# Kernel tuning notes

Measured on AMD Instinct MI355X. Metric: run time of the kernel, lower is better.

## Reference

```python
import jax, jax.numpy as jnp
import numpy as np

B, S, D = 4, 2048, 768   # batch, seq_len, dim_inp
H, E = 12, 64            # num_heads, dim_out (per-head)
LN_EPS = 1e-5


def setup_inputs() -> dict:
    key = jax.random.key(0)
    ks = jax.random.split(key, 12)
    sd = 1.0 / np.sqrt(D)
    x = jax.random.normal(ks[0], (B, S, D), dtype=jnp.float32)
    Wq = jax.random.normal(ks[1], (H, D, E), dtype=jnp.float32) * sd
    bq = jax.random.normal(ks[2], (H, E), dtype=jnp.float32) * 0.02
    Wk = jax.random.normal(ks[3], (H, D, E), dtype=jnp.float32) * sd
    bk = jax.random.normal(ks[4], (H, E), dtype=jnp.float32) * 0.02
    Wv = jax.random.normal(ks[5], (H, D, E), dtype=jnp.float32) * sd
    bv = jax.random.normal(ks[6], (H, E), dtype=jnp.float32) * 0.02
    Wo = jax.random.normal(ks[7], (H * E, D), dtype=jnp.float32) * (1.0 / np.sqrt(H * E))
    bo = jax.random.normal(ks[8], (D,), dtype=jnp.float32) * 0.02
    gamma = jnp.ones((D,), dtype=jnp.float32)
    beta = jnp.zeros((D,), dtype=jnp.float32)
    return {"input_tensor": x, "Wq": Wq, "bq": bq, "Wk": Wk, "bk": bk,
            "Wv": Wv, "bv": bv, "Wo": Wo, "bo": bo, "gamma": gamma, "beta": beta}


def reference(input_tensor, Wq, bq, Wk, bk, Wv, bv, Wo, bo, gamma, beta):
    x = input_tensor  # [B,S,D]
    # all heads at once: [B,H,S,E]
    q = jnp.einsum('bsd,hde->bhse', x, Wq) + bq[None, :, None, :]
    k = jnp.einsum('bsd,hde->bhse', x, Wk) + bk[None, :, None, :]
    v = jnp.einsum('bsd,hde->bhse', x, Wv) + bv[None, :, None, :]
    # NOTE: original divides by sqrt(seq_len) (query.size(1)), not sqrt(head_dim)
    scale = jnp.sqrt(jnp.float32(q.shape[2]))
    scores = jnp.einsum('bhse,bhte->bhst', q, k) / scale  # [B,H,S,S]
    attn = jax.nn.softmax(scores, axis=-1)
    ctx = jnp.einsum('bhst,bhte->bhse', attn, v)          # [B,H,S,E]
    # concat heads along last dim: [B,S,H*E]
    ctx = ctx.transpose(0, 2, 1, 3).reshape(x.shape[0], x.shape[1], -1)
    proj = ctx @ Wo + bo                                   # [B,S,D]
    h = x + proj
    mu = jnp.mean(h, axis=-1, keepdims=True)
    var = jnp.mean(jnp.square(h - mu), axis=-1, keepdims=True)
    y = (h - mu) * jax.lax.rsqrt(var + LN_EPS) * gamma + beta
    return y
```

## Files before the change

### kernel.cpp

```cpp
#include <hip/hip_runtime.h>


typedef __bf16 bf16x8 __attribute__((ext_vector_type(8)));
typedef __bf16 bf16x4 __attribute__((ext_vector_type(4)));
typedef float  f32x4  __attribute__((ext_vector_type(4)));
typedef float  f32x16 __attribute__((ext_vector_type(16)));
typedef unsigned u32x4 __attribute__((ext_vector_type(4)));

#define MFMA16(a,b,c) __builtin_amdgcn_mfma_f32_16x16x32_bf16((a),(b),(c),0,0,0)
#define MFMA32(a,b,c) __builtin_amdgcn_mfma_f32_32x32x16_bf16((a),(b),(c),0,0,0)
#define QSCALE2 (0.022097086912079612f * 1.4426950408889634f)

__device__ __forceinline__ void gload16(const void* g, void* l) {
  __builtin_amdgcn_global_load_lds((const __attribute__((address_space(1))) void*)g,
                                   (__attribute__((address_space(3))) void*)l, 16, 0, 0);
}

__global__ __launch_bounds__(256) void pack_kernel(
    const float* __restrict__ x, const float* __restrict__ Wq,
    const float* __restrict__ Wk, const float* __restrict__ Wv,
    const float* __restrict__ Wo,
    __bf16* __restrict__ xb, __bf16* __restrict__ wqkv, __bf16* __restrict__ wot) {
  int tid = blockIdx.x * 256 + threadIdx.x;
  int nth = gridDim.x * 256;
  for (int i = tid; i < 8192 * 768 / 4; i += nth) {
    float4 v = ((const float4*)x)[i];
    bf16x4 o; o[0] = (__bf16)v.x; o[1] = (__bf16)v.y; o[2] = (__bf16)v.z; o[3] = (__bf16)v.w;
    ((bf16x4*)xb)[i] = o;
  }
  for (int i = tid; i < 3 * 768 * 768; i += nth) {
    int n = i / 768, d = i - n * 768;
    int p = n / 768;
    int wn = n - p * 768;
    int h = wn >> 6, e = wn & 63;
    const float* W = (p == 0) ? Wq : (p == 1) ? Wk : Wv;
    wqkv[i] = (__bf16)W[(h * 768 + d) * 64 + e];
  }
  for (int i = tid; i < 768 * 768; i += nth) {
    int n = i / 768, k = i - n * 768;
    wot[i] = (__bf16)Wo[k * 768 + n];
  }
}

#define GEMM_CORE(A_, Bt_, m0_, n0_)                                              \
  __shared__ __bf16 As[128 * 32];                                                 \
  __shared__ __bf16 Bs[128 * 32];                                                 \
  const int tid = threadIdx.x;                                                    \
  const int w = tid >> 6, lane = tid & 63, ln = lane & 15, hi = lane >> 4;        \
  const int wr = w >> 1, wc = w & 1;                                              \
  f32x4 acc[4][4];                                                                \
  {                                                                               \
    f32x4 z = {0.f, 0.f, 0.f, 0.f};                                               \
    _Pragma("unroll") for (int i = 0; i < 4; ++i)                                 \
      _Pragma("unroll") for (int j = 0; j < 4; ++j) acc[i][j] = z;                \
  }                                                                               \
  {                                                                               \
    const int r0 = tid >> 2, cc = (tid & 3) * 8;                                  \
    const __bf16* ga0 = A_ + (size_t)(m0_ + r0) * 768 + cc;                       \
    const __bf16* ga1 = A_ + (size_t)(m0_ + 64 + r0) * 768 + cc;                  \
    const __bf16* gb0 = Bt_ + (size_t)(n0_ + r0) * 768 + cc;                      \
    const __bf16* gb1 = Bt_ + (size_t)(n0_ + 64 + r0) * 768 + cc;                 \
    __bf16* la0 = &As[w * 512];                                                   \
    __bf16* la1 = &As[2048 + w * 512];                                            \
    __bf16* lb0 = &Bs[w * 512];                                                   \
    __bf16* lb1 = &Bs[2048 + w * 512];                                            \
    for (int kt = 0; kt < 24; ++kt) {                                             \
      const int kk = kt * 32;                                                     \
      gload16(ga0 + kk, la0);                                                     \
      gload16(ga1 + kk, la1);                                                     \
      gload16(gb0 + kk, lb0);                                                     \
      gload16(gb1 + kk, lb1);                                                     \
      __syncthreads();                                                            \
      bf16x8 af[4], bfv[4];                                                       \
      _Pragma("unroll") for (int mt = 0; mt < 4; ++mt)                            \
        af[mt] = *(const bf16x8*)&As[(wr * 64 + mt * 16 + ln) * 32 + hi * 8];     \
      _Pragma("unroll") for (int nt = 0; nt < 4; ++nt)                            \
        bfv[nt] = *(const bf16x8*)&Bs[(wc * 64 + nt * 16 + ln) * 32 + hi * 8];    \
      _Pragma("unroll") for (int mt = 0; mt < 4; ++mt)                            \
        _Pragma("unroll") for (int nt = 0; nt < 4; ++nt)                          \
          acc[mt][nt] = MFMA16(af[mt], bfv[nt], acc[mt][nt]);                     \
      __syncthreads();                                                            \
    }                                                                             \
  }

__global__ __launch_bounds__(256) void gemm_qkv(
    const __bf16* __restrict__ A, const __bf16* __restrict__ Bt,
    const float* __restrict__ bq, const float* __restrict__ bk,
    const float* __restrict__ bv,
    __bf16* __restrict__ qb, __bf16* __restrict__ kb, __bf16* __restrict__ vt) {
  const int lin = blockIdx.y * 18 + blockIdx.x;
  const int swzb = (lin & 7) * 144 + (lin >> 3);
  const int m0 = (swzb / 18) * 128, n0 = (swzb % 18) * 128;
  GEMM_CORE(A, Bt, m0, n0)
  const int p = n0 / 768;
  const float* bias = (p == 0) ? bq : (p == 1) ? bk : bv;
  const float sc = (p == 0) ? QSCALE2 : 1.0f;
#pragma unroll
  for (int nt = 0; nt < 4; ++nt) {
    int n = n0 + wc * 64 + nt * 16 + ln;
    int wn = n - p * 768;
    int h = wn >> 6, e = wn & 63;
    float bb = bias[wn];
#pragma unroll
    for (int mt = 0; mt < 4; ++mt) {
      int mrow = m0 + wr * 64 + mt * 16 + hi * 4;
      int b = mrow >> 11, s0 = mrow & 2047;
      if (p == 2) {
        bf16x4 pk;
#pragma unroll
        for (int r = 0; r < 4; ++r) pk[r] = (__bf16)(acc[mt][nt][r] + bb);
        *(bf16x4*)&vt[(((size_t)b * 12 + h) * 64 + e) * 2048 + s0] = pk;
      } else {
        __bf16* dst = (p == 0) ? qb : kb;
#pragma unroll
        for (int r = 0; r < 4; ++r)
          dst[(((size_t)b * 12 + h) * 2048 + s0 + r) * 64 + e] =
              (__bf16)((acc[mt][nt][r] + bb) * sc);
      }
    }
  }
}

__global__ __launch_bounds__(256) void gemm_proj(
    const __bf16* __restrict__ A, const __bf16* __restrict__ Bt,
    const float* __restrict__ bo, const float* __restrict__ xres,
    float* __restrict__ hout) {
  const int lin = blockIdx.y * 6 + blockIdx.x;
  const int swzb = (lin & 7) * 48 + (lin >> 3);
  const int m0 = (swzb / 6) * 128, n0 = (swzb % 6) * 128;
  GEMM_CORE(A, Bt, m0, n0)
#pragma unroll
  for (int nt = 0; nt < 4; ++nt) {
    int n = n0 + wc * 64 + nt * 16 + ln;
    float bb = bo[n];
#pragma unroll
    for (int mt = 0; mt < 4; ++mt) {
      int mrow = m0 + wr * 64 + mt * 16 + hi * 4;
#pragma unroll
      for (int r = 0; r < 4; ++r) {
        size_t idx = (size_t)(mrow + r) * 768 + n;
        hout[idx] = acc[mt][nt][r] + bb + xres[idx];
      }
    }
  }
}

__global__ __launch_bounds__(256, 3) void attn_kernel(
    const __bf16* __restrict__ qb, const __bf16* __restrict__ kb,
    const __bf16* __restrict__ vt, __bf16* __restrict__ ctx) {
  __shared__ __align__(16) char lds[32768];
  const int tid = threadIdx.x;
  const int w = tid >> 6, lane = tid & 63;
  const int l31 = lane & 31, h = lane >> 5;
  const int lin = blockIdx.x * 16 + blockIdx.y;
  const int swzb = (lin & 7) * 96 + (lin >> 3);
  const int bh = swzb >> 4;
  const int q0 = (swzb & 15) * 128 + w * 32;

  const int o0 = tid * 16, o1 = o0 + 4096;
  const int r0s = o0 >> 7, cb0 = o0 & 127;
  const int r1s = o1 >> 7, cb1 = o1 & 127;
  const char* kgb = (const char*)(kb + (size_t)bh * 2048 * 64);
  const char* vgb = (const char*)(vt + (size_t)bh * 64 * 2048);
  const char* ksrc0 = kgb + r0s * 128 + (cb0 ^ ((r0s & 7) << 4));
  const char* ksrc1 = kgb + r1s * 128 + (cb1 ^ ((r1s & 7) << 4));
  const char* vsrc0 = vgb + r0s * 4096 + (cb0 ^ ((r0s & 7) << 4));
  const char* vsrc1 = vgb + r1s * 4096 + (cb1 ^ ((r1s & 7) << 4));
  char* kl0 = lds + w * 1024;
  char* vl0 = lds + 16384 + w * 1024;

#define STAGE(t_, b_) do {                                   \
    gload16(ksrc0 + (size_t)(t_) * 8192, kl0 + (b_) * 8192); \
    gload16(ksrc1 + (size_t)(t_) * 8192, kl0 + (b_) * 8192 + 4096); \
    gload16(vsrc0 + (size_t)(t_) * 128,  vl0 + (b_) * 8192); \
    gload16(vsrc1 + (size_t)(t_) * 128,  vl0 + (b_) * 8192 + 4096); \
  } while (0)

  const __bf16* qp = qb + ((size_t)bh * 2048 + q0 + l31) * 64 + h * 8;
  bf16x8 qf[4];
#pragma unroll
  for (int s = 0; s < 4; ++s) qf[s] = *(const bf16x8*)(qp + 16 * s);

  const int swz = (l31 & 7) << 4;
  const int krd = l31 * 128 + ((h * 16) ^ swz);
  const int vrd = 16384 + l31 * 128 + ((h * 16) ^ swz);

  float ls0 = 0.f, ls1 = 0.f, ls2 = 0.f, ls3 = 0.f;
  f32x16 cacc[2];
#pragma unroll
  for (int et = 0; et < 2; ++et)
#pragma unroll
    for (int r = 0; r < 16; ++r) cacc[et][r] = 0.f;

  STAGE(0, 0);
  __syncthreads();
  int buf = 0;

  for (int t = 0; t < 32; ++t) {
    if (t < 31) STAGE(t + 1, buf ^ 1);
    const char* kb_l = lds + buf * 8192;
    bf16x8 kf[2][4], vf[4][2];
#pragma unroll
    for (int kvt = 0; kvt < 2; ++kvt)
#pragma unroll
      for (int s = 0; s < 4; ++s)
        kf[kvt][s] = *(const bf16x8*)(kb_l + ((krd + kvt * 4096) ^ (s * 32)));
#pragma unroll
    for (int ks = 0; ks < 4; ++ks) {
      vf[ks][0] = *(const bf16x8*)(kb_l + ((vrd + 0 * 4096) ^ (ks * 32)));
      vf[ks][1] = *(const bf16x8*)(kb_l + ((vrd + 1 * 4096) ^ (ks * 32)));
    }
    u32x4 pau[4];
#pragma unroll
    for (int kvt = 0; kvt < 2; ++kvt) {
      f32x16 sa;
#pragma unroll
      for (int r = 0; r < 16; ++r) sa[r] = 0.f;
      __builtin_amdgcn_s_setprio(1);
#pragma unroll
      for (int s = 0; s < 4; ++s) sa = MFMA32(kf[kvt][s], qf[s], sa);
      __builtin_amdgcn_s_setprio(0);
      unsigned c0, c1, c2, c3, c4, c5, c6, c7;
#define PKPAIR(dst_, i_, ls_)                                                \
      {                                                                      \
        float pa_ = __builtin_amdgcn_exp2f(sa[2 * (i_)]);                    \
        float pb_ = __builtin_amdgcn_exp2f(sa[2 * (i_) + 1]);                \
        ls_ += pa_ + pb_;                                                    \
        asm("v_cvt_pk_bf16_f32 %0, %1, %2" : "=v"(dst_) : "v"(pa_), "v"(pb_)); \
      }
      PKPAIR(c0, 0, ls0) PKPAIR(c1, 1, ls1) PKPAIR(c2, 2, ls2) PKPAIR(c3, 3, ls3)
      PKPAIR(c4, 4, ls0) PKPAIR(c5, 5, ls1) PKPAIR(c6, 6, ls2) PKPAIR(c7, 7, ls3)
#undef PKPAIR
      asm("v_permlane32_swap_b32 %0, %1" : "+v"(c0), "+v"(c2));
      asm("v_permlane32_swap_b32 %0, %1" : "+v"(c1), "+v"(c3));
      asm("v_permlane32_swap_b32 %0, %1" : "+v"(c4), "+v"(c6));
      asm("v_permlane32_swap_b32 %0, %1" : "+v"(c5), "+v"(c7));
      pau[2 * kvt][0] = c0; pau[2 * kvt][1] = c1;
      pau[2 * kvt][2] = c2; pau[2 * kvt][3] = c3;
      pau[2 * kvt + 1][0] = c4; pau[2 * kvt + 1][1] = c5;
      pau[2 * kvt + 1][2] = c6; pau[2 * kvt + 1][3] = c7;
    }
    __builtin_amdgcn_s_setprio(1);
#pragma unroll
    for (int ks = 0; ks < 4; ++ks) {
      bf16x8 paf = __builtin_bit_cast(bf16x8, pau[ks]);
      cacc[0] = MFMA32(paf, vf[ks][0], cacc[0]);
      cacc[1] = MFMA32(paf, vf[ks][1], cacc[1]);
    }
    __builtin_amdgcn_s_setprio(0);
    __syncthreads();
    buf ^= 1;
  }
#undef STAGE

  float lsum = (ls0 + ls1) + (ls2 + ls3);
  lsum += __shfl_xor(lsum, 32, 64);
  float inv = 1.0f / lsum;
  const int b = bh / 12, hh = bh - b * 12;
#pragma unroll
  for (int r = 0; r < 16; ++r) {
    const int ql = (r & 3) + 8 * (r >> 2) + 4 * h;
    float rl = __shfl(inv, ql, 64);
    size_t base = ((size_t)b * 2048 + q0 + ql) * 768 + hh * 64 + l31;
    ctx[base]      = (__bf16)(cacc[0][r] * rl);
    ctx[base + 32] = (__bf16)(cacc[1][r] * rl);
  }
}

__global__ __launch_bounds__(256) void ln_kernel(
    const float* __restrict__ hb, const float* __restrict__ gamma,
    const float* __restrict__ beta, float* __restrict__ out) {
  __shared__ float ssum[4], ssq[4];
  const int row = blockIdx.x, t = threadIdx.x;
  const float* hr = hb + (size_t)row * 768;
  float v0 = hr[t], v1 = hr[t + 256], v2 = hr[t + 512];
  float sum = v0 + v1 + v2;
  float sq = v0 * v0 + v1 * v1 + v2 * v2;
#pragma unroll
  for (int mask = 1; mask < 64; mask <<= 1) {
    sum += __shfl_xor(sum, mask, 64);
    sq += __shfl_xor(sq, mask, 64);
  }
  const int w = t >> 6;
  if ((t & 63) == 0) { ssum[w] = sum; ssq[w] = sq; }
  __syncthreads();
  float s1 = ssum[0] + ssum[1] + ssum[2] + ssum[3];
  float s2 = ssq[0] + ssq[1] + ssq[2] + ssq[3];
  float mu = s1 * (1.0f / 768.0f);
  float var = s2 * (1.0f / 768.0f) - mu * mu;
  float rs = rsqrtf(var + 1e-5f);
  float* orow = out + (size_t)row * 768;
  orow[t]       = (v0 - mu) * rs * gamma[t]       + beta[t];
  orow[t + 256] = (v1 - mu) * rs * gamma[t + 256] + beta[t + 256];
  orow[t + 512] = (v2 - mu) * rs * gamma[t + 512] + beta[t + 512];
}

extern "C" void kernel_launch(void* const* d_in, const int* in_sizes, int n_in,
                              void* d_out, int out_size, void* d_ws, size_t ws_size,
                              hipStream_t stream) {
  const float* x     = (const float*)d_in[0];
  const float* Wq    = (const float*)d_in[1];
  const float* bq    = (const float*)d_in[2];
  const float* Wk    = (const float*)d_in[3];
  const float* bk    = (const float*)d_in[4];
  const float* Wv    = (const float*)d_in[5];
  const float* bv    = (const float*)d_in[6];
  const float* Wo    = (const float*)d_in[7];
  const float* bo    = (const float*)d_in[8];
  const float* gamma = (const float*)d_in[9];
  const float* beta  = (const float*)d_in[10];
  float* out = (float*)d_out;

  char* ws = (char*)d_ws;
  __bf16* xb   = (__bf16*)(ws);
  __bf16* wqkv = (__bf16*)(ws + 12582912);
  __bf16* wot  = (__bf16*)(ws + 16121856);
  __bf16* qb   = (__bf16*)(ws + 17301504);
  __bf16* kb   = (__bf16*)(ws + 29884416);
  __bf16* vt   = (__bf16*)(ws + 42467328);
  __bf16* ctx  = (__bf16*)(ws + 55050240);
  float*  hb   = (float*)(ws + 67633152);

  pack_kernel<<<dim3(1024), dim3(256), 0, stream>>>(x, Wq, Wk, Wv, Wo, xb, wqkv, wot);
  gemm_qkv<<<dim3(18, 64), dim3(256), 0, stream>>>(xb, wqkv, bq, bk, bv, qb, kb, vt);
  attn_kernel<<<dim3(48, 16), dim3(256), 0, stream>>>(qb, kb, vt, ctx);
  gemm_proj<<<dim3(6, 64), dim3(256), 0, stream>>>(ctx, wot, bo, x, hb);
  ln_kernel<<<dim3(8192), dim3(256), 0, stream>>>(hb, gamma, beta, out);
}
```

Baseline: 170.2 us.

## Compute softmax row sums via MFMA with ones and unroll tile loop by two

The attention kernel now accumulates softmax denominators by multiplying the bf16 probability tiles against a ones vector on the matrix cores, replacing the per-lane VALU adds and the final shuffle-based reduction. The KV loop is manually unrolled by two so the buffer index is a compile-time constant, and the LDS read offsets are precomputed. The block-index swizzle that spread work across XCDs is dropped in favour of the plain grid mapping. The extra MFMAs add matrix-core work each tile, and summing bf16-rounded probabilities slightly changes numerics.

Measured after the change: 166.5 us. -2.2%, faster.

```diff
diff --git a/kernel.cpp b/kernel.cpp
--- a/kernel.cpp
+++ b/kernel.cpp
@@ -152,10 +152,8 @@
   const int tid = threadIdx.x;
   const int w = tid >> 6, lane = tid & 63;
   const int l31 = lane & 31, h = lane >> 5;
-  const int lin = blockIdx.x * 16 + blockIdx.y;
-  const int swzb = (lin & 7) * 96 + (lin >> 3);
-  const int bh = swzb >> 4;
-  const int q0 = (swzb & 15) * 128 + w * 32;
+  const int bh = blockIdx.x;
+  const int q0 = blockIdx.y * 128 + w * 32;
 
   const int o0 = tid * 16, o1 = o0 + 4096;
   const int r0s = o0 >> 7, cb0 = o0 & 127;
@@ -184,83 +182,92 @@
   const int swz = (l31 & 7) << 4;
   const int krd = l31 * 128 + ((h * 16) ^ swz);
   const int vrd = 16384 + l31 * 128 + ((h * 16) ^ swz);
-
-  float ls0 = 0.f, ls1 = 0.f, ls2 = 0.f, ls3 = 0.f;
+  int ka_[8], va_[8];
+#pragma unroll
+  for (int kvt = 0; kvt < 2; ++kvt)
+#pragma unroll
+    for (int s = 0; s < 4; ++s) ka_[kvt * 4 + s] = (krd + kvt * 4096) ^ (s * 32);
+#pragma unroll
+  for (int ks = 0; ks < 4; ++ks)
+#pragma unroll
+    for (int et = 0; et < 2; ++et) va_[ks * 2 + et] = (vrd + et * 4096) ^ (ks * 32);
+
+  f32x16 FZ;
+#pragma unroll
+  for (int r = 0; r < 16; ++r) FZ[r] = 0.f;
+  bf16x8 onesf;
+#pragma unroll
+  for (int j = 0; j < 8; ++j) onesf[j] = (__bf16)1.0f;
+
+  f32x16 lacc = FZ;
   f32x16 cacc[2];
-#pragma unroll
-  for (int et = 0; et < 2; ++et)
-#pragma unroll
-    for (int r = 0; r < 16; ++r) cacc[et][r] = 0.f;
+  cacc[0] = FZ; cacc[1] = FZ;
 
   STAGE(0, 0);
   __syncthreads();
-  int buf = 0;
-
-  for (int t = 0; t < 32; ++t) {
-    if (t < 31) STAGE(t + 1, buf ^ 1);
-    const char* kb_l = lds + buf * 8192;
-    bf16x8 kf[2][4], vf[4][2];
-#pragma unroll
-    for (int kvt = 0; kvt < 2; ++kvt)
-#pragma unroll
-      for (int s = 0; s < 4; ++s)
-        kf[kvt][s] = *(const bf16x8*)(kb_l + ((krd + kvt * 4096) ^ (s * 32)));
-#pragma unroll
-    for (int ks = 0; ks < 4; ++ks) {
-      vf[ks][0] = *(const bf16x8*)(kb_l + ((vrd + 0 * 4096) ^ (ks * 32)));
-      vf[ks][1] = *(const bf16x8*)(kb_l + ((vrd + 1 * 4096) ^ (ks * 32)));
-    }
-    u32x4 pau[4];
-#pragma unroll
-    for (int kvt = 0; kvt < 2; ++kvt) {
-      f32x16 sa;
-#pragma unroll
-      for (int r = 0; r < 16; ++r) sa[r] = 0.f;
-      __builtin_amdgcn_s_setprio(1);
-#pragma unroll
-      for (int s = 0; s < 4; ++s) sa = MFMA32(kf[kvt][s], qf[s], sa);
-      __builtin_amdgcn_s_setprio(0);
-      unsigned c0, c1, c2, c3, c4, c5, c6, c7;
-#define PKPAIR(dst_, i_, ls_)                                                \
-      {                                                                      \
-        float pa_ = __builtin_amdgcn_exp2f(sa[2 * (i_)]);                    \
-        float pb_ = __builtin_amdgcn_exp2f(sa[2 * (i_) + 1]);                \
-        ls_ += pa_ + pb_;                                                    \
-        asm("v_cvt_pk_bf16_f32 %0, %1, %2" : "=v"(dst_) : "v"(pa_), "v"(pb_)); \
-      }
-      PKPAIR(c0, 0, ls0) PKPAIR(c1, 1, ls1) PKPAIR(c2, 2, ls2) PKPAIR(c3, 3, ls3)
-      PKPAIR(c4, 4, ls0) PKPAIR(c5, 5, ls1) PKPAIR(c6, 6, ls2) PKPAIR(c7, 7, ls3)
+
+#define PKPAIR(dst_, i_)                                                       \
+  {                                                                            \
+    float pa_ = __builtin_amdgcn_exp2f(sa[2 * (i_)]);                          \
+    float pb_ = __builtin_amdgcn_exp2f(sa[2 * (i_) + 1]);                      \
+    asm("v_cvt_pk_bf16_f32 %0, %1, %2" : "=v"(dst_) : "v"(pa_), "v"(pb_));     \
+  }
+
+#define TILEBODY(B_, T_)                                                       \
+  {                                                                            \
+    if ((T_) < 31) STAGE((T_) + 1, (B_) ^ 1);                                  \
+    bf16x8 kf[2][4], vf[4][2];                                                 \
+    _Pragma("unroll") for (int kvt = 0; kvt < 2; ++kvt)                        \
+      _Pragma("unroll") for (int s = 0; s < 4; ++s)                            \
+        kf[kvt][s] = *(const bf16x8*)(lds + (B_) * 8192 + ka_[kvt * 4 + s]);   \
+    _Pragma("unroll") for (int ks = 0; ks < 4; ++ks)                           \
+      _Pragma("unroll") for (int et = 0; et < 2; ++et)                         \
+        vf[ks][et] = *(const bf16x8*)(lds + (B_) * 8192 + va_[ks * 2 + et]);   \
+    u32x4 pau[4];                                                              \
+    _Pragma("unroll") for (int kvt = 0; kvt < 2; ++kvt) {                      \
+      __builtin_amdgcn_s_setprio(1);                                           \
+      f32x16 sa = MFMA32(kf[kvt][0], qf[0], FZ);                               \
+      sa = MFMA32(kf[kvt][1], qf[1], sa);                                      \
+      sa = MFMA32(kf[kvt][2], qf[2], sa);                                      \
+      sa = MFMA32(kf[kvt][3], qf[3], sa);                                      \
+      __builtin_amdgcn_s_setprio(0);                                           \
+      unsigned c0, c1, c2, c3, c4, c5, c6, c7;                                 \
+      PKPAIR(c0, 0) PKPAIR(c1, 1) PKPAIR(c2, 2) PKPAIR(c3, 3)                  \
+      PKPAIR(c4, 4) PKPAIR(c5, 5) PKPAIR(c6, 6) PKPAIR(c7, 7)                  \
+      asm("v_permlane32_swap_b32 %0, %1" : "+v"(c0), "+v"(c2));                \
+      asm("v_permlane32_swap_b32 %0, %1" : "+v"(c1), "+v"(c3));                \
+      asm("v_permlane32_swap_b32 %0, %1" : "+v"(c4), "+v"(c6));                \
+      asm("v_permlane32_swap_b32 %0, %1" : "+v"(c5), "+v"(c7));                \
+      pau[2 * kvt][0] = c0; pau[2 * kvt][1] = c1;                              \
+      pau[2 * kvt][2] = c2; pau[2 * kvt][3] = c3;                              \
+      pau[2 * kvt + 1][0] = c4; pau[2 * kvt + 1][1] = c5;                      \
+      pau[2 * kvt + 1][2] = c6; pau[2 * kvt + 1][3] = c7;                      \
+      lacc = MFMA32(__builtin_bit_cast(bf16x8, pau[2 * kvt]), onesf, lacc);    \
+      lacc = MFMA32(__builtin_bit_cast(bf16x8, pau[2 * kvt + 1]), onesf, lacc);\
+    }                                                                          \
+    __builtin_amdgcn_s_setprio(1);                                             \
+    _Pragma("unroll") for (int ks = 0; ks < 4; ++ks) {                         \
+      bf16x8 paf = __builtin_bit_cast(bf16x8, pau[ks]);                        \
+      cacc[0] = MFMA32(paf, vf[ks][0], cacc[0]);                               \
+      cacc[1] = MFMA32(paf, vf[ks][1], cacc[1]);                               \
+    }                                                                          \
+    __builtin_amdgcn_s_setprio(0);                                             \
+    __syncthreads();                                                           \
+  }
+
+  for (int t = 0; t < 32; t += 2) {
+    TILEBODY(0, t)
+    TILEBODY(1, t + 1)
+  }
+#undef TILEBODY
 #undef PKPAIR
-      asm("v_permlane32_swap_b32 %0, %1" : "+v"(c0), "+v"(c2));
-      asm("v_permlane32_swap_b32 %0, %1" : "+v"(c1), "+v"(c3));
-      asm("v_permlane32_swap_b32 %0, %1" : "+v"(c4), "+v"(c6));
-      asm("v_permlane32_swap_b32 %0, %1" : "+v"(c5), "+v"(c7));
-      pau[2 * kvt][0] = c0; pau[2 * kvt][1] = c1;
-      pau[2 * kvt][2] = c2; pau[2 * kvt][3] = c3;
-      pau[2 * kvt + 1][0] = c4; pau[2 * kvt + 1][1] = c5;
-      pau[2 * kvt + 1][2] = c6; pau[2 * kvt + 1][3] = c7;
-    }
-    __builtin_amdgcn_s_setprio(1);
-#pragma unroll
-    for (int ks = 0; ks < 4; ++ks) {
-      bf16x8 paf = __builtin_bit_cast(bf16x8, pau[ks]);
-      cacc[0] = MFMA32(paf, vf[ks][0], cacc[0]);
-      cacc[1] = MFMA32(paf, vf[ks][1], cacc[1]);
-    }
-    __builtin_amdgcn_s_setprio(0);
-    __syncthreads();
-    buf ^= 1;
-  }
 #undef STAGE
 
-  float lsum = (ls0 + ls1) + (ls2 + ls3);
-  lsum += __shfl_xor(lsum, 32, 64);
-  float inv = 1.0f / lsum;
   const int b = bh / 12, hh = bh - b * 12;
 #pragma unroll
   for (int r = 0; r < 16; ++r) {
     const int ql = (r & 3) + 8 * (r >> 2) + 4 * h;
-    float rl = __shfl(inv, ql, 64);
+    float rl = __builtin_amdgcn_rcpf(lacc[r]);
     size_t base = ((size_t)b * 2048 + q0 + ql) * 768 + hh * 64 + l31;
     ctx[base]      = (__bf16)(cacc[0][r] * rl);
     ctx[base + 32] = (__bf16)(cacc[1][r] * rl);
```

## Drop LDS staging in attention; load K/V directly and compute row sums via MFMA

Applied to the files above, without the earlier changes.

The attention kernel no longer stages K and V tiles through double-buffered LDS with barriers. Each wave now reads its K/V fragments straight from global memory, relying on L1/L2 caching. The softmax row sum is computed by extra MFMAs against a vector of ones, which replaces the scalar exp accumulation and the shuffle-based reduction. The block-index swizzle is also removed. This trades away LDS sharing, so each of the four waves fetches the same K/V redundantly, and it adds MFMA work in exchange for removing syncs and VALU adds.

Measured after the change: 273.4 us. 1.61x slower.

```diff
diff --git a/kernel.cpp b/kernel.cpp
--- a/kernel.cpp
+++ b/kernel.cpp
@@ -148,89 +148,64 @@
 __global__ __launch_bounds__(256, 3) void attn_kernel(
     const __bf16* __restrict__ qb, const __bf16* __restrict__ kb,
     const __bf16* __restrict__ vt, __bf16* __restrict__ ctx) {
-  __shared__ __align__(16) char lds[32768];
   const int tid = threadIdx.x;
   const int w = tid >> 6, lane = tid & 63;
   const int l31 = lane & 31, h = lane >> 5;
-  const int lin = blockIdx.x * 16 + blockIdx.y;
-  const int swzb = (lin & 7) * 96 + (lin >> 3);
-  const int bh = swzb >> 4;
-  const int q0 = (swzb & 15) * 128 + w * 32;
-
-  const int o0 = tid * 16, o1 = o0 + 4096;
-  const int r0s = o0 >> 7, cb0 = o0 & 127;
-  const int r1s = o1 >> 7, cb1 = o1 & 127;
-  const char* kgb = (const char*)(kb + (size_t)bh * 2048 * 64);
-  const char* vgb = (const char*)(vt + (size_t)bh * 64 * 2048);
-  const char* ksrc0 = kgb + r0s * 128 + (cb0 ^ ((r0s & 7) << 4));
-  const char* ksrc1 = kgb + r1s * 128 + (cb1 ^ ((r1s & 7) << 4));
-  const char* vsrc0 = vgb + r0s * 4096 + (cb0 ^ ((r0s & 7) << 4));
-  const char* vsrc1 = vgb + r1s * 4096 + (cb1 ^ ((r1s & 7) << 4));
-  char* kl0 = lds + w * 1024;
-  char* vl0 = lds + 16384 + w * 1024;
-
-#define STAGE(t_, b_) do {                                   \
-    gload16(ksrc0 + (size_t)(t_) * 8192, kl0 + (b_) * 8192); \
-    gload16(ksrc1 + (size_t)(t_) * 8192, kl0 + (b_) * 8192 + 4096); \
-    gload16(vsrc0 + (size_t)(t_) * 128,  vl0 + (b_) * 8192); \
-    gload16(vsrc1 + (size_t)(t_) * 128,  vl0 + (b_) * 8192 + 4096); \
-  } while (0)
+  const int bh = blockIdx.x;
+  const int q0 = blockIdx.y * 128 + w * 32;
 
   const __bf16* qp = qb + ((size_t)bh * 2048 + q0 + l31) * 64 + h * 8;
   bf16x8 qf[4];
 #pragma unroll
   for (int s = 0; s < 4; ++s) qf[s] = *(const bf16x8*)(qp + 16 * s);
 
-  const int swz = (l31 & 7) << 4;
-  const int krd = l31 * 128 + ((h * 16) ^ swz);
-  const int vrd = 16384 + l31 * 128 + ((h * 16) ^ swz);
-
-  float ls0 = 0.f, ls1 = 0.f, ls2 = 0.f, ls3 = 0.f;
+  const char* kp0 = (const char*)kb + (size_t)bh * 262144 + l31 * 128 + 16 * h;
+  const char* kp1 = kp0 + 4096;
+  const char* vp0 = (const char*)vt + (size_t)bh * 262144 + l31 * 4096 + 16 * h;
+  const char* vp1 = vp0 + 131072;
+
+  f32x16 FZ;
+#pragma unroll
+  for (int r = 0; r < 16; ++r) FZ[r] = 0.f;
+  bf16x8 onesf;
+#pragma unroll
+  for (int j = 0; j < 8; ++j) onesf[j] = (__bf16)1.0f;
+
+  f32x16 lacc = FZ;
   f32x16 cacc[2];
-#pragma unroll
-  for (int et = 0; et < 2; ++et)
-#pragma unroll
-    for (int r = 0; r < 16; ++r) cacc[et][r] = 0.f;
-
-  STAGE(0, 0);
-  __syncthreads();
-  int buf = 0;
+  cacc[0] = FZ; cacc[1] = FZ;
+
+#define PKPAIR(dst_, i_)                                                       \
+  {                                                                            \
+    float pa_ = __builtin_amdgcn_exp2f(sa[2 * (i_)]);                          \
+    float pb_ = __builtin_amdgcn_exp2f(sa[2 * (i_) + 1]);                      \
+    asm("v_cvt_pk_bf16_f32 %0, %1, %2" : "=v"(dst_) : "v"(pa_), "v"(pb_));     \
+  }
 
   for (int t = 0; t < 32; ++t) {
-    if (t < 31) STAGE(t + 1, buf ^ 1);
-    const char* kb_l = lds + buf * 8192;
     bf16x8 kf[2][4], vf[4][2];
 #pragma unroll
-    for (int kvt = 0; kvt < 2; ++kvt)
-#pragma unroll
-      for (int s = 0; s < 4; ++s)
-        kf[kvt][s] = *(const bf16x8*)(kb_l + ((krd + kvt * 4096) ^ (s * 32)));
+    for (int s = 0; s < 4; ++s) {
+      kf[0][s] = *(const bf16x8*)(kp0 + s * 32);
+      kf[1][s] = *(const bf16x8*)(kp1 + s * 32);
+    }
 #pragma unroll
     for (int ks = 0; ks < 4; ++ks) {
-      vf[ks][0] = *(const bf16x8*)(kb_l + ((vrd + 0 * 4096) ^ (ks * 32)));
-      vf[ks][1] = *(const bf16x8*)(kb_l + ((vrd + 1 * 4096) ^ (ks * 32)));
+      vf[ks][0] = *(const bf16x8*)(vp0 + ks * 32);
+      vf[ks][1] = *(const bf16x8*)(vp1 + ks * 32);
     }
     u32x4 pau[4];
 #pragma unroll
     for (int kvt = 0; kvt < 2; ++kvt) {
-      f32x16 sa;
-#pragma unroll
-      for (int r = 0; r < 16; ++r) sa[r] = 0.f;
       __builtin_amdgcn_s_setprio(1);
-#pragma unroll
-      for (int s = 0; s < 4; ++s) sa = MFMA32(kf[kvt][s], qf[s], sa);
+      f32x16 sa = MFMA32(kf[kvt][0], qf[0], FZ);
+      sa = MFMA32(kf[kvt][1], qf[1], sa);
+      sa = MFMA32(kf[kvt][2], qf[2], sa);
+      sa = MFMA32(kf[kvt][3], qf[3], sa);
       __builtin_amdgcn_s_setprio(0);
       unsigned c0, c1, c2, c3, c4, c5, c6, c7;
-#define PKPAIR(dst_, i_, ls_)                                                \
-      {                                                                      \
-        float pa_ = __builtin_amdgcn_exp2f(sa[2 * (i_)]);                    \
-        float pb_ = __builtin_amdgcn_exp2f(sa[2 * (i_) + 1]);                \
-        ls_ += pa_ + pb_;                                                    \
-        asm("v_cvt_pk_bf16_f32 %0, %1, %2" : "=v"(dst_) : "v"(pa_), "v"(pb_)); \
-      }
-      PKPAIR(c0, 0, ls0) PKPAIR(c1, 1, ls1) PKPAIR(c2, 2, ls2) PKPAIR(c3, 3, ls3)
-      PKPAIR(c4, 4, ls0) PKPAIR(c5, 5, ls1) PKPAIR(c6, 6, ls2) PKPAIR(c7, 7, ls3)
-#undef PKPAIR
+      PKPAIR(c0, 0) PKPAIR(c1, 1) PKPAIR(c2, 2) PKPAIR(c3, 3)
+      PKPAIR(c4, 4) PKPAIR(c5, 5) PKPAIR(c6, 6) PKPAIR(c7, 7)
       asm("v_permlane32_swap_b32 %0, %1" : "+v"(c0), "+v"(c2));
       asm("v_permlane32_swap_b32 %0, %1" : "+v"(c1), "+v"(c3));
       asm("v_permlane32_swap_b32 %0, %1" : "+v"(c4), "+v"(c6));
@@ -239,6 +214,8 @@
       pau[2 * kvt][2] = c2; pau[2 * kvt][3] = c3;
       pau[2 * kvt + 1][0] = c4; pau[2 * kvt + 1][1] = c5;
       pau[2 * kvt + 1][2] = c6; pau[2 * kvt + 1][3] = c7;
+      lacc = MFMA32(__builtin_bit_cast(bf16x8, pau[2 * kvt]), onesf, lacc);
+      lacc = MFMA32(__builtin_bit_cast(bf16x8, pau[2 * kvt + 1]), onesf, lacc);
     }
     __builtin_amdgcn_s_setprio(1);
 #pragma unroll
@@ -248,19 +225,15 @@
       cacc[1] = MFMA32(paf, vf[ks][1], cacc[1]);
     }
     __builtin_amdgcn_s_setprio(0);
-    __syncthreads();
-    buf ^= 1;
-  }
-#undef STAGE
-
-  float lsum = (ls0 + ls1) + (ls2 + ls3);
-  lsum += __shfl_xor(lsum, 32, 64);
-  float inv = 1.0f / lsum;
+    kp0 += 8192; kp1 += 8192; vp0 += 128; vp1 += 128;
+  }
+#undef PKPAIR
+
   const int b = bh / 12, hh = bh - b * 12;
 #pragma unroll
   for (int r = 0; r < 16; ++r) {
     const int ql = (r & 3) + 8 * (r >> 2) + 4 * h;
-    float rl = __shfl(inv, ql, 64);
+    float rl = __builtin_amdgcn_rcpf(lacc[r]);
     size_t base = ((size_t)b * 2048 + q0 + ql) * 768 + hh * 64 + l31;
     ctx[base]      = (__bf16)(cacc[0][r] * rl);
     ctx[base + 32] = (__bf16)(cacc[1][r] * rl);
```
